# Kernel tuning notes

Measured on AMD Instinct MI355X. Metric: run time of the kernel, lower is better.

Reference implementation:

```python
import jax, jax.numpy as jnp
import numpy as np

N_NODES = 100000
N_EDGES = 3200000
IN_DIM = 256
OUT_DIM = 64


def setup_inputs() -> dict:
    key = jax.random.key(0)
    k1, k2, k3 = jax.random.split(key, 3)
    h = jax.random.normal(k1, (N_NODES, IN_DIM), dtype=jnp.float32)
    W = jax.random.normal(k2, (IN_DIM, OUT_DIM), dtype=jnp.float32) * (IN_DIM ** -0.5)
    b = jnp.zeros((OUT_DIM,), dtype=jnp.float32)
    edges = jax.random.randint(k3, (2, N_EDGES), 0, N_NODES, dtype=jnp.int64)
    return {"h": h, "W": W, "b": b, "edges": edges}


def reference(h, W, b, edges):
    # DGL GraphConv, norm='both':
    #   out = D_dst^{-1/2} * A * (D_src^{-1/2} * (h @ W)) + b
    # degrees clamped to min 1; then log_softmax over classes.
    N = h.shape[0]
    src, dst = edges[0], edges[1]
    ones = jnp.ones(src.shape, dtype=h.dtype)
    out_deg = jax.ops.segment_sum(ones, src, num_segments=N)
    in_deg = jax.ops.segment_sum(ones, dst, num_segments=N)
    norm_src = jnp.maximum(out_deg, 1.0) ** -0.5  # [N]
    norm_dst = jnp.maximum(in_deg, 1.0) ** -0.5   # [N]
    # in_dim > out_dim: project first (matches DGL's mult-first optimization)
    m = (h @ W) * norm_src[:, None]               # [N, out_dim]
    agg = jax.ops.segment_sum(m[src], dst, num_segments=N)  # SpMM
    out = agg * norm_dst[:, None] + b
    return jax.nn.log_softmax(out, axis=1)
```

## Files before the change

kernel.cpp:

```cpp
#include <hip/hip_runtime.h>
#include <hip/hip_fp16.h>
#include <math.h>

#define IN_DIM 256
#define OUT_DIM 64
#define BROWS 256
#define GROWS 128
#define SC_THREADS 512
#define SC_EPB 16
#define SC_EDGES (SC_THREADS * SC_EPB)
#define BM 128
#define KC2 64
#define LDH 68
#define CSR_CAP 5120

typedef _Float16 f16x4 __attribute__((ext_vector_type(4)));
typedef float f32x4 __attribute__((ext_vector_type(4)));

__global__ void __launch_bounds__(SC_THREADS) scatter_pairs_kernel(
        const int* __restrict__ src, const int* __restrict__ dst,
        int* __restrict__ dcursor, int* __restrict__ scursor,
        unsigned* __restrict__ pairs, unsigned char* __restrict__ sbytes,
        int n_edges, int nb, int cap) {
    __shared__ int lhd[512];
    __shared__ int lbd[512];
    __shared__ int lod[512];
    __shared__ int lhs[512];
    __shared__ int lbs[512];
    __shared__ int los[512];
    __shared__ unsigned stp[SC_EDGES];
    __shared__ unsigned char stb[SC_EDGES];

    const int t = threadIdx.x;
    const int wave = t >> 6;
    const int lane = t & 63;

    lhd[t] = 0; lhs[t] = 0;
    __syncthreads();

    const int base = blockIdx.x * SC_EDGES;
    int s[SC_EPB], d[SC_EPB];
    if (base + SC_EDGES <= n_edges) {
        const int4* s4 = (const int4*)(src + base);
        const int4* d4 = (const int4*)(dst + base);
        #pragma unroll
        for (int j = 0; j < SC_EPB / 4; ++j) {
            int4 a = s4[j * SC_THREADS + t];
            int4 c = d4[j * SC_THREADS + t];
            s[4*j+0] = a.x; s[4*j+1] = a.y; s[4*j+2] = a.z; s[4*j+3] = a.w;
            d[4*j+0] = c.x; d[4*j+1] = c.y; d[4*j+2] = c.z; d[4*j+3] = c.w;
        }
        #pragma unroll
        for (int i = 0; i < SC_EPB; ++i) {
            atomicAdd(&lhd[d[i] >> 8], 1);
            atomicAdd(&lhs[s[i] >> 8], 1);
        }
    } else {
        #pragma unroll
        for (int i = 0; i < SC_EPB; ++i) {
            int e = base + i * SC_THREADS + t;
            if (e < n_edges) {
                s[i] = src[e];
                d[i] = dst[e];
                atomicAdd(&lhd[d[i] >> 8], 1);
                atomicAdd(&lhs[s[i] >> 8], 1);
            } else {
                s[i] = -1; d[i] = 0;
            }
        }
    }
    __syncthreads();

    for (int i = t; i < nb; i += SC_THREADS) {
        int c = lhd[i];
        lbd[i] = c ? atomicAdd(&dcursor[i], c) : 0;
        c = lhs[i];
        lbs[i] = c ? atomicAdd(&scursor[i], c) : 0;
    }

    {
        int vd = (t < nb) ? lhd[t] : 0;
        int vs = (t < nb) ? lhs[t] : 0;
        lod[t] = vd; los[t] = vs;
        __syncthreads();
        #pragma unroll
        for (int dd = 1; dd < 512; dd <<= 1) {
            int td = (t >= dd) ? lod[t - dd] : 0;
            int ts = (t >= dd) ? los[t - dd] : 0;
            __syncthreads();
            lod[t] += td; los[t] += ts;
            __syncthreads();
        }
        lod[t] -= vd; los[t] -= vs;
    }
    __syncthreads();

    #pragma unroll
    for (int i = 0; i < SC_EPB; ++i) {
        if (s[i] >= 0) {
            int bkt = d[i] >> 8;
            int pos = atomicAdd(&lod[bkt], 1);
            stp[pos] = ((unsigned)s[i] << 8) | (unsigned)(d[i] & 255);
            int sb = s[i] >> 8;
            int spos = atomicAdd(&los[sb], 1);
            stb[spos] = (unsigned char)(s[i] & 255);
        }
    }
    __syncthreads();

    for (int b2 = wave; b2 < nb; b2 += SC_THREADS / 64) {
        int cnt = lhd[b2];
        if (cnt) {
            int st = lod[b2] - cnt;
            int gb = lbd[b2];
            unsigned* gp = pairs + (size_t)b2 * cap;
            for (int j = lane; j < cnt; j += 64)
                if (gb + j < cap) gp[gb + j] = stp[st + j];
        }
        cnt = lhs[b2];
        if (cnt) {
            int st = los[b2] - cnt;
            int gb = lbs[b2];
            unsigned char* gp = sbytes + (size_t)b2 * cap;
            for (int j = lane; j < cnt; j += 64)
                if (gb + j < cap) gp[gb + j] = stb[st + j];
        }
    }
}

__global__ void __launch_bounds__(256) count_src_kernel(
        const unsigned char* __restrict__ sbytes, const int* __restrict__ scursor,
        int* __restrict__ out_deg, int n_nodes, int cap) {
    __shared__ int cnt[BROWS];
    cnt[threadIdx.x] = 0;
    __syncthreads();
    const int beg = blockIdx.x * cap;
    int len = scursor[blockIdx.x];
    if (len > cap) len = cap;
    const int end = beg + len;
    for (int i = beg + threadIdx.x; i < end; i += 256)
        atomicAdd(&cnt[sbytes[i]], 1);
    __syncthreads();
    const int row = blockIdx.x * BROWS + threadIdx.x;
    if (row < n_nodes) out_deg[row] = cnt[threadIdx.x];
}

__global__ void __launch_bounds__(256) gemm_kernel(
        const float* __restrict__ h, const float* __restrict__ W,
        const int* __restrict__ out_deg, __half* __restrict__ m, int n_nodes) {
    __shared__ _Float16 hs[BM * LDH];
    __shared__ _Float16 Wt[OUT_DIM * LDH];

    const int t = threadIdx.x;
    const int wave = t >> 6;
    const int lane = t & 63;
    const int lg = lane >> 4;
    const int li = lane & 15;
    const int rowBase = blockIdx.x * BM;

    f32x4 acc[2][4];
    #pragma unroll
    for (int rt = 0; rt < 2; ++rt)
        #pragma unroll
        for (int ct = 0; ct < 4; ++ct)
            acc[rt][ct] = (f32x4){0.f, 0.f, 0.f, 0.f};

    for (int kc = 0; kc < IN_DIM / KC2; ++kc) {
        __syncthreads();
        #pragma unroll
        for (int i = 0; i < 8; ++i) {
            int idx = t + 256 * i;
            int row = idx >> 4;
            int s4 = idx & 15;
            float4 v = make_float4(0.f, 0.f, 0.f, 0.f);
            if (rowBase + row < n_nodes)
                v = *(const float4*)(h + (size_t)(rowBase + row) * IN_DIM
                                     + kc * KC2 + s4 * 4);
            _Float16* dp = &hs[row * LDH + s4 * 4];
            dp[0] = (_Float16)v.x; dp[1] = (_Float16)v.y;
            dp[2] = (_Float16)v.z; dp[3] = (_Float16)v.w;
        }
        #pragma unroll
        for (int i = 0; i < 16; ++i) {
            int idx = t + 256 * i;
            int k = idx >> 6;
            int n = idx & 63;
            Wt[n * LDH + k] = (_Float16)W[(size_t)(kc * KC2 + k) * OUT_DIM + n];
        }
        __syncthreads();

        #pragma unroll
        for (int ks = 0; ks < KC2 / 16; ++ks) {
            const int k0 = ks * 16 + lg * 4;
            f16x4 b0 = *(const f16x4*)&hs[((wave * 2 + 0) * 16 + li) * LDH + k0];
            f16x4 b1 = *(const f16x4*)&hs[((wave * 2 + 1) * 16 + li) * LDH + k0];
            f16x4 a0 = *(const f16x4*)&Wt[(0 * 16 + li) * LDH + k0];
            f16x4 a1 = *(const f16x4*)&Wt[(1 * 16 + li) * LDH + k0];
            f16x4 a2 = *(const f16x4*)&Wt[(2 * 16 + li) * LDH + k0];
            f16x4 a3 = *(const f16x4*)&Wt[(3 * 16 + li) * LDH + k0];
            acc[0][0] = __builtin_amdgcn_mfma_f32_16x16x16f16(a0, b0, acc[0][0], 0, 0, 0);
            acc[0][1] = __builtin_amdgcn_mfma_f32_16x16x16f16(a1, b0, acc[0][1], 0, 0, 0);
            acc[0][2] = __builtin_amdgcn_mfma_f32_16x16x16f16(a2, b0, acc[0][2], 0, 0, 0);
            acc[0][3] = __builtin_amdgcn_mfma_f32_16x16x16f16(a3, b0, acc[0][3], 0, 0, 0);
            acc[1][0] = __builtin_amdgcn_mfma_f32_16x16x16f16(a0, b1, acc[1][0], 0, 0, 0);
            acc[1][1] = __builtin_amdgcn_mfma_f32_16x16x16f16(a1, b1, acc[1][1], 0, 0, 0);
            acc[1][2] = __builtin_amdgcn_mfma_f32_16x16x16f16(a2, b1, acc[1][2], 0, 0, 0);
            acc[1][3] = __builtin_amdgcn_mfma_f32_16x16x16f16(a3, b1, acc[1][3], 0, 0, 0);
        }
    }

    #pragma unroll
    for (int rt = 0; rt < 2; ++rt) {
        int row = rowBase + (wave * 2 + rt) * 16 + li;
        if (row < n_nodes) {
            float nr = rsqrtf(fmaxf((float)out_deg[row], 1.0f));
            #pragma unroll
            for (int ct = 0; ct < 4; ++ct) {
                f32x4 dv = acc[rt][ct];
                union { __half2 h2[2]; uint2 u; } pk;
                pk.h2[0] = __floats2half2_rn(dv[0] * nr, dv[1] * nr);
                pk.h2[1] = __floats2half2_rn(dv[2] * nr, dv[3] * nr);
                *(uint2*)(m + (size_t)row * OUT_DIM + ct * 16 + lg * 4) = pk.u;
            }
        }
    }
}

__global__ void __launch_bounds__(512) bucket_gather_kernel(
        const unsigned* __restrict__ pairs, const int* __restrict__ dcursor,
        const __half* __restrict__ m, const float* __restrict__ b,
        float* __restrict__ out, int n_nodes, int cap) {
    __shared__ int cnt[GROWS];
    __shared__ int rofs[GROWS];
    __shared__ int cur[GROWS];
    __shared__ int csr[CSR_CAP];

    const int t = threadIdx.x;
    const int bkt = blockIdx.x >> 1;
    const int hsel = blockIdx.x & 1;
    const unsigned hbit = (unsigned)hsel << 7;
    const int beg = bkt * cap;
    int len = dcursor[bkt];
    if (len > cap) len = cap;
    const int end = beg + len;
    const int rowBase = bkt * BROWS + hsel * GROWS;

    const int wave = t >> 6;
    const int lane = t & 63;
    const int half = lane >> 5;
    const int c    = lane & 31;
    const __half2* __restrict__ m2 = (const __half2*)m;
    const float2 bb = *(const float2*)(b + 2 * c);

    if (t < GROWS) cnt[t] = 0;
    __syncthreads();

    for (int i = beg + t; i < end; i += 512) {
        unsigned p = pairs[i];
        if ((p & 128u) == hbit) atomicAdd(&cnt[p & 127u], 1);
    }
    __syncthreads();
    if (t < GROWS) rofs[t] = cnt[t];
    __syncthreads();
    #pragma unroll
    for (int d = 1; d < GROWS; d <<= 1) {
        int tv = (t < GROWS && t >= d) ? rofs[t - d] : 0;
        __syncthreads();
        if (t < GROWS) rofs[t] += tv;
        __syncthreads();
    }
    if (t < GROWS) cur[t] = rofs[t] - cnt[t];
    __syncthreads();
    const int tot = rofs[GROWS - 1];

    if (tot <= CSR_CAP) {
        for (int i = beg + t; i < end; i += 512) {
            unsigned p = pairs[i];
            if ((p & 128u) == hbit) {
                int pos = atomicAdd(&cur[p & 127u], 1);
                csr[pos] = (int)(p >> 8);
            }
        }
        __syncthreads();
        for (int r = wave; r < GROWS; r += 8) {
            const int row = rowBase + r;
            if (row >= n_nodes) continue;
            const int cend = rofs[r];
            const int cbeg = cend - cnt[r];
            float ax = 0.f, ay = 0.f;
            int i = cbeg;
            for (; i + 16 <= cend; i += 16) {
                int s[8];
                #pragma unroll
                for (int k = 0; k < 8; ++k) s[k] = csr[i + 2 * k + half];
                #pragma unroll
                for (int k = 0; k < 8; ++k) {
                    float2 f = __half22float2(m2[(unsigned)(s[k] * (OUT_DIM / 2) + c)]);
                    ax += f.x; ay += f.y;
                }
            }
            for (int e = i + half; e < cend; e += 2) {
                float2 f = __half22float2(m2[(unsigned)(csr[e] * (OUT_DIM / 2) + c)]);
                ax += f.x; ay += f.y;
            }
            ax += __shfl_xor(ax, 32, 64);
            ay += __shfl_xor(ay, 32, 64);

            float nd = rsqrtf(fmaxf((float)cnt[r], 1.0f));
            float x0 = ax * nd + bb.x;
            float x1 = ay * nd + bb.y;
            float mx = fmaxf(x0, x1);
            #pragma unroll
            for (int o = 16; o > 0; o >>= 1) mx = fmaxf(mx, __shfl_xor(mx, o, 64));
            float ex0 = expf(x0 - mx), ex1 = expf(x1 - mx);
            float sm = ex0 + ex1;
            #pragma unroll
            for (int o = 16; o > 0; o >>= 1) sm += __shfl_xor(sm, o, 64);
            float ls = logf(sm);
            if (half == 0)
                *(float2*)(out + (size_t)row * OUT_DIM + 2 * c) =
                    make_float2(x0 - mx - ls, x1 - mx - ls);
        }
    } else {
        for (int r = wave; r < GROWS; r += 8) {
            const int row = rowBase + r;
            if (row >= n_nodes) continue;
            const unsigned match = (unsigned)(hsel * GROWS + r);
            float ax = 0.f, ay = 0.f;
            for (int e = beg; e < end; ++e) {
                unsigned p = pairs[e];
                if ((p & 255u) == match) {
                    float2 f = __half22float2(m2[(unsigned)((p >> 8) * (OUT_DIM / 2) + c)]);
                    ax += f.x; ay += f.y;
                }
            }
            float nd = rsqrtf(fmaxf((float)cnt[r], 1.0f));
            float x0 = ax * nd + bb.x;
            float x1 = ay * nd + bb.y;
            float mx = fmaxf(x0, x1);
            #pragma unroll
            for (int o = 16; o > 0; o >>= 1) mx = fmaxf(mx, __shfl_xor(mx, o, 64));
            float ex0 = expf(x0 - mx), ex1 = expf(x1 - mx);
            float sm = ex0 + ex1;
            #pragma unroll
            for (int o = 16; o > 0; o >>= 1) sm += __shfl_xor(sm, o, 64);
            float ls = logf(sm);
            if (half == 0)
                *(float2*)(out + (size_t)row * OUT_DIM + 2 * c) =
                    make_float2(x0 - mx - ls, x1 - mx - ls);
        }
    }
}

static inline size_t align16(size_t x) { return (x + 15) & ~(size_t)15; }

extern "C" void kernel_launch(void* const* d_in, const int* in_sizes, int n_in,
                              void* d_out, int out_size, void* d_ws, size_t ws_size,
                              hipStream_t stream) {
    const float* h = (const float*)d_in[0];
    const float* W = (const float*)d_in[1];
    const float* b = (const float*)d_in[2];
    const int* edges = (const int*)d_in[3];

    const int out_dim = in_sizes[2];
    const int in_dim  = in_sizes[1] / out_dim;
    const int n_nodes = in_sizes[0] / in_dim;
    const int n_edges = in_sizes[3] / 2;

    const int* src = edges;
    const int* dst = edges + n_edges;

    float* out = (float*)d_out;

    const int nb = (n_nodes + BROWS - 1) / BROWS;

    const int epb = (n_edges + nb - 1) / nb;
    const int cap = (epb + (epb >> 2) + 1023 + 1023) & ~1023;

    char* ws = (char*)d_ws;
    size_t off = 0;
    int* out_deg     = (int*)(ws + off); off = align16(off + (size_t)n_nodes * 4);
    int* dcursor     = (int*)(ws + off); off = align16(off + (size_t)nb * 4);
    int* scursor     = (int*)(ws + off); off = align16(off + (size_t)nb * 4);
    __half* m        = (__half*)(ws + off); off = align16(off + (size_t)n_nodes * OUT_DIM * 2);
    unsigned* pairs  = (unsigned*)(ws + off); off = align16(off + (size_t)nb * cap * 4);
    unsigned char* sbytes = (unsigned char*)m;

    (void)hipMemsetAsync(dcursor, 0,
                         (size_t)((char*)(scursor + nb) - (char*)dcursor), stream);

    const int sc_blocks = (n_edges + SC_EDGES - 1) / SC_EDGES;

    scatter_pairs_kernel<<<sc_blocks, SC_THREADS, 0, stream>>>(
        src, dst, dcursor, scursor, pairs, sbytes, n_edges, nb, cap);
    count_src_kernel<<<nb, 256, 0, stream>>>(sbytes, scursor, out_deg, n_nodes, cap);

    gemm_kernel<<<(n_nodes + BM - 1) / BM, 256, 0, stream>>>(h, W, out_deg, m, n_nodes);

    bucket_gather_kernel<<<2 * nb, 512, 0, stream>>>(pairs, dcursor, m, b, out,
                                                     n_nodes, cap);
}
```

Baseline: 358.8 us.

## Slice gather CSR by source-node range so all block waves hit the same m region together

The gather kernel's per-row CSR is subdivided into 8 slices keyed by the high bits of the source index, giving a 1024-key counting sort. Each wave now walks all its 16 rows slice by slice, keeping 16 accumulator pairs in registers, and processes two rows at once to add memory-level parallelism. The aim is to confine concurrent random reads of the fp16 m table to a narrower address window and improve L2/MALL hit rate. In exchange the prefix scan is longer, register pressure is higher, and rows shorter than the old 16-wide unrolled loop may see less load batching.

```diff
diff --git a/kernel.cpp b/kernel.cpp
--- a/kernel.cpp
+++ b/kernel.cpp
@@ -13,6 +13,8 @@
 #define KC2 64
 #define LDH 68
 #define CSR_CAP 5120
+#define NSLICE 8
+#define NKEY (GROWS * NSLICE)
 
 typedef _Float16 f16x4 __attribute__((ext_vector_type(4)));
 typedef float f32x4 __attribute__((ext_vector_type(4)));
@@ -230,9 +232,9 @@
         const unsigned* __restrict__ pairs, const int* __restrict__ dcursor,
         const __half* __restrict__ m, const float* __restrict__ b,
         float* __restrict__ out, int n_nodes, int cap) {
-    __shared__ int cnt[GROWS];
-    __shared__ int rofs[GROWS];
-    __shared__ int cur[GROWS];
+    __shared__ int cnt[NKEY];
+    __shared__ int rofs[NKEY];
+    __shared__ int cur[NKEY];
     __shared__ int csr[CSR_CAP];
 
     const int t = threadIdx.x;
@@ -252,63 +254,115 @@
     const __half2* __restrict__ m2 = (const __half2*)m;
     const float2 bb = *(const float2*)(b + 2 * c);
 
-    if (t < GROWS) cnt[t] = 0;
+    cnt[t] = 0; cnt[t + 512] = 0;
     __syncthreads();
 
     for (int i = beg + t; i < end; i += 512) {
         unsigned p = pairs[i];
-        if ((p & 128u) == hbit) atomicAdd(&cnt[p & 127u], 1);
-    }
-    __syncthreads();
-    if (t < GROWS) rofs[t] = cnt[t];
+        if ((p & 128u) == hbit)
+            atomicAdd(&cnt[(int)(p & 127u) * NSLICE + (int)((p >> 22) & 7u)], 1);
+    }
+    __syncthreads();
+    rofs[t] = cnt[t]; rofs[t + 512] = cnt[t + 512];
     __syncthreads();
     #pragma unroll
-    for (int d = 1; d < GROWS; d <<= 1) {
-        int tv = (t < GROWS && t >= d) ? rofs[t - d] : 0;
-        __syncthreads();
-        if (t < GROWS) rofs[t] += tv;
-        __syncthreads();
-    }
-    if (t < GROWS) cur[t] = rofs[t] - cnt[t];
-    __syncthreads();
-    const int tot = rofs[GROWS - 1];
+    for (int d = 1; d < NKEY; d <<= 1) {
+        int v1 = (t >= d) ? rofs[t - d] : 0;
+        int v2 = rofs[t + 512 - d];
+        __syncthreads();
+        rofs[t] += v1; rofs[t + 512] += v2;
+        __syncthreads();
+    }
+    cur[t] = rofs[t] - cnt[t];
+    cur[t + 512] = rofs[t + 512] - cnt[t + 512];
+    __syncthreads();
+    const int tot = rofs[NKEY - 1];
 
     if (tot <= CSR_CAP) {
         for (int i = beg + t; i < end; i += 512) {
             unsigned p = pairs[i];
             if ((p & 128u) == hbit) {
-                int pos = atomicAdd(&cur[p & 127u], 1);
+                int key = (int)(p & 127u) * NSLICE + (int)((p >> 22) & 7u);
+                int pos = atomicAdd(&cur[key], 1);
                 csr[pos] = (int)(p >> 8);
             }
         }
         __syncthreads();
+        float ax[16], ay[16];
+        #pragma unroll
+        for (int j = 0; j < 16; ++j) { ax[j] = 0.f; ay[j] = 0.f; }
+
+        for (int s = 0; s < NSLICE; ++s) {
+            #pragma unroll 2
+            for (int j = 0; j < 16; j += 2) {
+                const int kA = (wave + 8 * j) * NSLICE + s;
+                const int kB = (wave + 8 * (j + 1)) * NSLICE + s;
+                const int eA = rofs[kA]; int iA = eA - cnt[kA] + half;
+                const int eB = rofs[kB]; int iB = eB - cnt[kB] + half;
+                float axA = 0.f, ayA = 0.f, axB = 0.f, ayB = 0.f;
+                while (iA < eA && iB < eB) {
+                    int sA = csr[iA], sB = csr[iB];
+                    float2 fA = __half22float2(m2[(unsigned)(sA * (OUT_DIM / 2) + c)]);
+                    float2 fB = __half22float2(m2[(unsigned)(sB * (OUT_DIM / 2) + c)]);
+                    axA += fA.x; ayA += fA.y;
+                    axB += fB.x; ayB += fB.y;
+                    iA += 2; iB += 2;
+                }
+                for (; iA < eA; iA += 2) {
+                    float2 f = __half22float2(m2[(unsigned)(csr[iA] * (OUT_DIM / 2) + c)]);
+                    axA += f.x; ayA += f.y;
+                }
+                for (; iB < eB; iB += 2) {
+                    float2 f = __half22float2(m2[(unsigned)(csr[iB] * (OUT_DIM / 2) + c)]);
+                    axB += f.x; ayB += f.y;
+                }
+                ax[j] += axA; ay[j] += ayA;
+                ax[j + 1] += axB; ay[j + 1] += ayB;
+            }
+        }
+
+        #pragma unroll 1
+        for (int j = 0; j < 16; ++j) {
+            const int r = wave + 8 * j;
+            const int row = rowBase + r;
+            float axv = ax[j], ayv = ay[j];
+            axv += __shfl_xor(axv, 32, 64);
+            ayv += __shfl_xor(ayv, 32, 64);
+            const int deg = rofs[r * NSLICE + NSLICE - 1]
+                          - (rofs[r * NSLICE] - cnt[r * NSLICE]);
+            float nd = rsqrtf(fmaxf((float)deg, 1.0f));
+            float x0 = axv * nd + bb.x;
+            float x1 = ayv * nd + bb.y;
+            float mx = fmaxf(x0, x1);
+            #pragma unroll
+            for (int o = 16; o > 0; o >>= 1) mx = fmaxf(mx, __shfl_xor(mx, o, 64));
+            float ex0 = expf(x0 - mx), ex1 = expf(x1 - mx);
+            float sm = ex0 + ex1;
+            #pragma unroll
+            for (int o = 16; o > 0; o >>= 1) sm += __shfl_xor(sm, o, 64);
+            float ls = logf(sm);
+            if (half == 0 && row < n_nodes)
+                *(float2*)(out + (size_t)row * OUT_DIM + 2 * c) =
+                    make_float2(x0 - mx - ls, x1 - mx - ls);
+        }
+    } else {
         for (int r = wave; r < GROWS; r += 8) {
             const int row = rowBase + r;
             if (row >= n_nodes) continue;
-            const int cend = rofs[r];
-            const int cbeg = cend - cnt[r];
-            float ax = 0.f, ay = 0.f;
-            int i = cbeg;
-            for (; i + 16 <= cend; i += 16) {
-                int s[8];
-                #pragma unroll
-                for (int k = 0; k < 8; ++k) s[k] = csr[i + 2 * k + half];
-                #pragma unroll
-                for (int k = 0; k < 8; ++k) {
-                    float2 f = __half22float2(m2[(unsigned)(s[k] * (OUT_DIM / 2) + c)]);
-                    ax += f.x; ay += f.y;
+            const unsigned match = (unsigned)(hsel * GROWS + r);
+            float axv = 0.f, ayv = 0.f;
+            for (int e = beg; e < end; ++e) {
+                unsigned p = pairs[e];
+                if ((p & 255u) == match) {
+                    float2 f = __half22float2(m2[(unsigned)((p >> 8) * (OUT_DIM / 2) + c)]);
+                    axv += f.x; ayv += f.y;
                 }
             }
-            for (int e = i + half; e < cend; e += 2) {
-                float2 f = __half22float2(m2[(unsigned)(csr[e] * (OUT_DIM / 2) + c)]);
-                ax += f.x; ay += f.y;
-            }
-            ax += __shfl_xor(ax, 32, 64);
-            ay += __shfl_xor(ay, 32, 64);
-
-            float nd = rsqrtf(fmaxf((float)cnt[r], 1.0f));
-            float x0 = ax * nd + bb.x;
-            float x1 = ay * nd + bb.y;
+            const int deg = rofs[r * NSLICE + NSLICE - 1]
+                          - (rofs[r * NSLICE] - cnt[r * NSLICE]);
+            float nd = rsqrtf(fmaxf((float)deg, 1.0f));
+            float x0 = axv * nd + bb.x;
+            float x1 = ayv * nd + bb.y;
             float mx = fmaxf(x0, x1);
             #pragma unroll
             for (int o = 16; o > 0; o >>= 1) mx = fmaxf(mx, __shfl_xor(mx, o, 64));
@@ -321,34 +375,6 @@
                 *(float2*)(out + (size_t)row * OUT_DIM + 2 * c) =
                     make_float2(x0 - mx - ls, x1 - mx - ls);
         }
-    } else {
-        for (int r = wave; r < GROWS; r += 8) {
-            const int row = rowBase + r;
-            if (row >= n_nodes) continue;
-            const unsigned match = (unsigned)(hsel * GROWS + r);
-            float ax = 0.f, ay = 0.f;
-            for (int e = beg; e < end; ++e) {
-                unsigned p = pairs[e];
-                if ((p & 255u) == match) {
-                    float2 f = __half22float2(m2[(unsigned)((p >> 8) * (OUT_DIM / 2) + c)]);
-                    ax += f.x; ay += f.y;
-                }
-            }
-            float nd = rsqrtf(fmaxf((float)cnt[r], 1.0f));
-            float x0 = ax * nd + bb.x;
-            float x1 = ay * nd + bb.y;
-            float mx = fmaxf(x0, x1);
-            #pragma unroll
-            for (int o = 16; o > 0; o >>= 1) mx = fmaxf(mx, __shfl_xor(mx, o, 64));
-            float ex0 = expf(x0 - mx), ex1 = expf(x1 - mx);
-            float sm = ex0 + ex1;
-            #pragma unroll
-            for (int o = 16; o > 0; o >>= 1) sm += __shfl_xor(sm, o, 64);
-            float ls = logf(sm);
-            if (half == 0)
-                *(float2*)(out + (size_t)row * OUT_DIM + 2 * c) =
-                    make_float2(x0 - mx - ls, x1 - mx - ls);
-        }
     }
 }
 
```

Result: slower. 375.8 us (+4.7%).
